# Optimization experiments

Measured on AMD Instinct MI355X. Metric: run time of the kernel, lower is better.

The kernel has to match this reference:

```python
import jax, jax.numpy as jnp
import numpy as np
from jax import lax

B, CIN, COUT, H, W = 4, 256, 256, 64, 64
KH = KW = 3
STRIDE = PAD = DIL = 1
GROUPS = 1
K = KH * KW
HO = (H + 2 * PAD - DIL * (KH - 1) - 1) // STRIDE + 1
WO = (W + 2 * PAD - DIL * (KW - 1) - 1) // STRIDE + 1
DN = ('NCHW', 'OIHW', 'NCHW')


def _sep_conv(x, dw, pw):
    # Separable2d: depthwise kxk conv (stride/pad/dilation) then pointwise 1x1.
    y = lax.conv_general_dilated(x, dw, (STRIDE, STRIDE), [(PAD, PAD), (PAD, PAD)],
                                 rhs_dilation=(DIL, DIL), feature_group_count=x.shape[1],
                                 dimension_numbers=DN)
    return lax.conv_general_dilated(y, pw, (1, 1), 'VALID', dimension_numbers=DN)


def _deform_conv2d(x, offset, mask, weight, bias):
    Bb, Cin, Hh, Ww = x.shape
    O = weight.shape[0]
    G = offset.shape[1] // (2 * K)  # offset groups
    offs = offset.reshape(Bb, G, K, 2, HO, WO)
    dy, dx = offs[:, :, :, 0], offs[:, :, :, 1]  # [B,G,K,Ho,Wo]
    ki, kj = jnp.meshgrid(jnp.arange(KH), jnp.arange(KW), indexing='ij')
    base_y = (-PAD + ki.reshape(K, 1) * DIL + jnp.arange(HO)[None, :] * STRIDE).astype(x.dtype)  # [K,Ho]
    base_x = (-PAD + kj.reshape(K, 1) * DIL + jnp.arange(WO)[None, :] * STRIDE).astype(x.dtype)  # [K,Wo]
    py = base_y[None, None, :, :, None] + dy  # [B,G,K,Ho,Wo]
    px = base_x[None, None, :, None, :] + dx

    xg = x.reshape(Bb, G, Cin // G, Hh, Ww)

    def bilinear(img, py, px):
        # img [C,H,W], py/px [K,Ho,Wo]; zero-padding outside bounds.
        y0 = jnp.floor(py)
        x0 = jnp.floor(px)
        out = jnp.zeros((img.shape[0],) + py.shape, img.dtype)
        for a, (iy, wy) in enumerate((((y0), (y0 + 1 - py)), ((y0 + 1), (py - y0)))):
            for b, (ix, wx) in enumerate((((x0), (x0 + 1 - px)), ((x0 + 1), (px - x0)))):
                valid = (iy >= 0) & (iy < Hh) & (ix >= 0) & (ix < Ww)
                iyc = jnp.clip(iy, 0, Hh - 1).astype(jnp.int32)
                ixc = jnp.clip(ix, 0, Ww - 1).astype(jnp.int32)
                v = img[:, iyc, ixc]  # [C,K,Ho,Wo]
                out = out + v * (wy * wx * valid)[None]
        return out

    sampled = jax.vmap(jax.vmap(bilinear))(xg, py, px)  # [B,G,C/G,K,Ho,Wo]
    m = mask.reshape(Bb, G, K, HO, WO)
    sampled = sampled * m[:, :, None]

    cols = sampled.reshape(Bb, Cin, K, HO, WO).reshape(Bb, GROUPS, Cin // GROUPS, K, HO, WO)
    wr = weight.reshape(GROUPS, O // GROUPS, Cin // GROUPS, K)
    out = jnp.einsum('bgckhw,gock->bgohw', cols, wr).reshape(Bb, O, HO, WO)
    return out + bias[None, :, None, None]


def setup_inputs() -> dict:
    key = jax.random.key(0)
    ks = jax.random.split(key, 7)
    x = jax.random.normal(ks[0], (B, CIN, H, W), jnp.float32)
    weight = jax.random.normal(ks[1], (COUT, CIN // GROUPS, KH, KW), jnp.float32) / np.sqrt(CIN * K)
    bias = jax.random.normal(ks[2], (COUT,), jnp.float32) * 0.01
    off_dw = jax.random.normal(ks[3], (CIN, 1, KH, KW), jnp.float32) * 0.01
    off_pw = jax.random.normal(ks[4], (2 * K * GROUPS, CIN, 1, 1), jnp.float32) * 0.01
    mask_dw = jax.random.normal(ks[5], (CIN, 1, KH, KW), jnp.float32) * 0.01
    mask_pw = jax.random.normal(ks[6], (K * GROUPS, CIN, 1, 1), jnp.float32) * 0.01
    return dict(x=x, weight=weight, bias=bias, off_dw=off_dw, off_pw=off_pw,
                mask_dw=mask_dw, mask_pw=mask_pw)


def reference(x, weight, bias, off_dw, off_pw, mask_dw, mask_pw):
    offset = _sep_conv(x, off_dw, off_pw)                       # [B,2*K,Ho,Wo]
    mask = jax.nn.sigmoid(_sep_conv(x, mask_dw, mask_pw)) * 2.0  # MaskSigmoid(scale=2)
    return _deform_conv2d(x, offset, mask, weight, bias)
```

## Files before the change

kernel.cpp:

```cpp
#include <hip/hip_runtime.h>

#define CIN   256
#define COUT  256
#define HH    64
#define WW    64
#define KD    2304
#define NPIX  16384
#define SPLIT 16
#define CPS   (CIN / SPLIT)
#define NSTEP 36

typedef __attribute__((ext_vector_type(4))) float  float4v;
typedef __attribute__((ext_vector_type(2))) unsigned int uint2v;
typedef _Float16 h2 __attribute__((ext_vector_type(2)));
typedef _Float16 h8 __attribute__((ext_vector_type(8)));
typedef unsigned int u32;
typedef unsigned short u16;

__device__ __forceinline__ h2 as_h2(u32 v) { union { u32 u; h2 h; } x; x.u = v; return x.h; }
__device__ __forceinline__ u32 as_u32(h2 h) { union { u32 u; h2 h; } x; x.h = h; return x.u; }
__device__ __forceinline__ u16 f2h_bits(float f) { _Float16 h = (_Float16)f; return *(u16*)&h; }

__device__ __forceinline__ void gload_lds16(const void* g, void* l) {
  __builtin_amdgcn_global_load_lds((const __attribute__((address_space(1))) u32*)g,
                                   (__attribute__((address_space(3))) u32*)l, 16, 0, 0);
}

__global__ __launch_bounds__(256) void offmask_part_kernel(
    const float* __restrict__ x,
    const float* __restrict__ off_dw, const float* __restrict__ off_pw,
    const float* __restrict__ mask_dw, const float* __restrict__ mask_pw,
    float* __restrict__ part)
{
  int m = blockIdx.x * 256 + threadIdx.x;
  int s = blockIdx.y;
  int b = m >> 12, pix = m & 4095;
  int ho = pix >> 6, wo = pix & 63;
  const float* xb = x + (size_t)b * CIN * 4096;

  float acc[27];
#pragma unroll
  for (int j = 0; j < 27; ++j) acc[j] = 0.f;

  int c0 = s * CPS;
  for (int ci = 0; ci < CPS; ++ci) {
    int c = c0 + ci;
    const float* xc = xb + (size_t)c * 4096;
    float d_off = 0.f, d_msk = 0.f;
#pragma unroll
    for (int t = 0; t < 9; ++t) {
      int gy = ho + t / 3 - 1, gx = wo + t % 3 - 1;
      bool ok = (gy >= 0) & (gy < HH) & (gx >= 0) & (gx < WW);
      float v = ok ? xc[gy * 64 + gx] : 0.f;
      d_off += v * off_dw[c * 9 + t];
      d_msk += v * mask_dw[c * 9 + t];
    }
#pragma unroll
    for (int j = 0; j < 18; ++j) acc[j] += d_off * off_pw[j * 256 + c];
#pragma unroll
    for (int j = 0; j < 9; ++j) acc[18 + j] += d_msk * mask_pw[j * 256 + c];
  }
  float* pp = part + ((size_t)s * NPIX + m) * 32;
#pragma unroll
  for (int j = 0; j < 27; ++j) pp[j] = acc[j];
}

__global__ __launch_bounds__(256) void offmask_reduce_kernel(
    const float* __restrict__ part, float* __restrict__ rec)
{
  int i = blockIdx.x * 256 + threadIdx.x;
  int m = i >> 5, j = i & 31;
  if (j >= 27) { rec[i] = 0.f; return; }
  float sum = 0.f;
#pragma unroll
  for (int s = 0; s < SPLIT; ++s) sum += part[((size_t)s * NPIX + m) * 32 + j];
  rec[i] = (j < 18) ? sum : 2.f / (1.f + __expf(-sum));
}

__global__ __launch_bounds__(256) void wconv_kernel(const float* __restrict__ w,
                                                    u16* __restrict__ wb)
{
  int i = blockIdx.x * 256 + threadIdx.x;
  int co = i / KD, rem = i - co * KD;
  int c = rem / 9, kk = rem - c * 9;
  wb[co * KD + kk * 256 + c] = f2h_bits(w[i]);
}

__global__ __launch_bounds__(256) void xpose_kernel(const float* __restrict__ x,
                                                    u16* __restrict__ xt)
{
  __shared__ float t[64][65];
  int ptile = blockIdx.x;
  int ctile = blockIdx.y;
  int b     = blockIdx.z;
  int tid = threadIdx.x;
  const float* xb = x + (size_t)b * CIN * 4096 + (size_t)ctile * 64 * 4096 + ptile * 64;
#pragma unroll
  for (int i = 0; i < 16; ++i) {
    int c = i * 4 + (tid >> 6), p = tid & 63;
    t[c][p] = xb[(size_t)c * 4096 + p];
  }
  __syncthreads();
  u16* xo = xt + ((size_t)b * 4096 + ptile * 64) * 256 + ctile * 64;
#pragma unroll
  for (int i = 0; i < 16; ++i) {
    int p = i * 4 + (tid >> 6), c = tid & 63;
    xo[(size_t)p * 256 + c] = f2h_bits(t[c][p]);
  }
}

__global__ __launch_bounds__(512, 4) void gemm_fused_kernel(
    const u16* __restrict__ A,
    const u16* __restrict__ xt,
    const float* __restrict__ rec,
    const float* __restrict__ bias,
    float* __restrict__ out,
    float* __restrict__ tmp)
{
  __shared__ __align__(16) u16 lA[3][256 * 32];
  __shared__ __align__(16) u16 lB[2][64 * 32];
  const int tid = threadIdx.x;
  const int bid = blockIdx.x;
  const int h   = bid & 1;
  const int ptile = bid >> 1;
  const int m0  = ptile * 64;
  const int b_img = ptile >> 6;
  const int cbase = h * 128;
  const int wave = tid >> 6, lane = tid & 63;
  const int wm = wave >> 1, wn = wave & 1;
  const int rl = lane & 15, kq = lane >> 4;
  const int sA = (kq ^ (rl & 3) ^ ((rl >> 2) & 3)) * 8;

  const int rA  = tid >> 2;
  const int koA = ((tid & 3) ^ (rA & 3) ^ ((rA >> 2) & 3)) * 8;
  const u16* aRow0 = A + (size_t)rA * KD + koA;
  const u16* aRow1 = A + (size_t)(rA + 128) * KD + koA;

  const int spx = tid >> 3;
  const int sc4 = (tid & 7) * 4;
  const int m_px = m0 + spx;
  const int ho = (m_px & 4095) >> 6, wo = m_px & 63;
  const float* rp = rec + (size_t)m_px * 32;
  const u16* xb = xt + (size_t)b_img * 4096 * 256;
  const int wAddr = spx * 32 +
                    ((((tid >> 1) & 3) ^ ((spx & 3) ^ ((spx >> 2) & 3))) * 8) +
                    (tid & 1) * 4;

  u32 cOff[4];
  h2  wh[4];

#define KCOL(t_) (((t_) >> 2) * 256 + cbase + ((t_) & 3) * 32)

#define CALC_CORNERS(kk_) do {                                             \
    float dy = rp[(kk_) * 2], dx = rp[(kk_) * 2 + 1], msk = rp[18 + (kk_)];\
    float py  = (float)(ho - 1 + ((kk_) / 3)) + dy;                        \
    float pxf = (float)(wo - 1 + ((kk_) % 3)) + dx;                        \
    float fy = floorf(py), fx = floorf(pxf);                               \
    int y0 = (int)fy, x0 = (int)fx;                                        \
    float wy1 = py - fy, wy0 = 1.f - wy1;                                  \
    float wx1 = pxf - fx, wx0 = 1.f - wx1;                                 \
    _Pragma("unroll")                                                      \
    for (int cr = 0; cr < 4; ++cr) {                                       \
      int iy = y0 + (cr >> 1), ix = x0 + (cr & 1);                         \
      bool valid = (iy >= 0) & (iy < HH) & (ix >= 0) & (ix < WW);          \
      int iyc = min(max(iy, 0), HH - 1), ixc = min(max(ix, 0), WW - 1);    \
      cOff[cr] = (u32)(iyc * 64 + ixc) * 256;                              \
      float wy = (cr >> 1) ? wy1 : wy0;                                    \
      float wx = (cr & 1) ? wx1 : wx0;                                     \
      float wf = valid ? (wy * wx * msk) : 0.f;                            \
      _Float16 hw = (_Float16)wf;                                          \
      wh[cr] = (h2){hw, hw};                                               \
    }                                                                      \
  } while (0)

#define STAGE_A(k_, slot_) do {                                            \
    int k0_ = KCOL(k_);                                                    \
    gload_lds16(aRow0 + k0_, lA[slot_] + tid * 8);                         \
    gload_lds16(aRow1 + k0_, lA[slot_] + (tid + 512) * 8);                 \
  } while (0)

#define BLEND_WRITE(bufi_, v0_, v1_, v2_, v3_) do {                        \
    h2 a01 = wh[0] * as_h2((v0_)[0]) + wh[1] * as_h2((v1_)[0]);            \
    a01   += wh[2] * as_h2((v2_)[0]) + wh[3] * as_h2((v3_)[0]);            \
    h2 a23 = wh[0] * as_h2((v0_)[1]) + wh[1] * as_h2((v1_)[1]);            \
    a23   += wh[2] * as_h2((v2_)[1]) + wh[3] * as_h2((v3_)[1]);            \
    uint2v wv; wv[0] = as_u32(a01); wv[1] = as_u32(a23);                   \
    *(uint2v*)&lB[bufi_][wAddr] = wv;                                      \
  } while (0)

  float4v acc[4][2];
#pragma unroll
  for (int m = 0; m < 4; ++m)
#pragma unroll
    for (int n = 0; n < 2; ++n) acc[m][n] = float4v{0.f, 0.f, 0.f, 0.f};

  {
    CALC_CORNERS(0);
    int c0n = cbase + sc4;
    uint2v v0 = *(const uint2v*)(xb + cOff[0] + c0n);
    uint2v v1 = *(const uint2v*)(xb + cOff[1] + c0n);
    uint2v v2 = *(const uint2v*)(xb + cOff[2] + c0n);
    uint2v v3 = *(const uint2v*)(xb + cOff[3] + c0n);
    STAGE_A(0, 0);
    STAGE_A(1, 1);
    asm volatile("s_waitcnt vmcnt(2)" ::: "memory");
    BLEND_WRITE(0, v0, v1, v2, v3);
    asm volatile("s_waitcnt lgkmcnt(0)" ::: "memory");
    __builtin_amdgcn_s_barrier();
  }

  for (int it = 0; it < 6; ++it) {
#pragma unroll
    for (int u = 0; u < 6; ++u) {
      const int t = it * 6 + u;
      const int tn  = (t + 1 == NSTEP) ? 0 : t + 1;
      const int tn2 = (t + 2 >= NSTEP) ? (t + 2 - NSTEP) : t + 2;
      if ((tn & 3) == 0) CALC_CORNERS(tn >> 2);
      int c0n = cbase + (tn & 3) * 32 + sc4;
      uint2v v0 = *(const uint2v*)(xb + cOff[0] + c0n);
      uint2v v1 = *(const uint2v*)(xb + cOff[1] + c0n);
      uint2v v2 = *(const uint2v*)(xb + cOff[2] + c0n);
      uint2v v3 = *(const uint2v*)(xb + cOff[3] + c0n);
      STAGE_A(tn2, (u + 2) % 3);
      h8 af[4], bf[2];
#pragma unroll
      for (int m = 0; m < 4; ++m)
        af[m] = *(const h8*)&lA[u % 3][(wm * 64 + m * 16 + rl) * 32 + sA];
#pragma unroll
      for (int n = 0; n < 2; ++n)
        bf[n] = *(const h8*)&lB[u & 1][(wn * 32 + n * 16 + rl) * 32 + sA];
#pragma unroll
      for (int m = 0; m < 4; ++m)
#pragma unroll
        for (int n = 0; n < 2; ++n)
          acc[m][n] = __builtin_amdgcn_mfma_f32_16x16x32_f16(af[m], bf[n], acc[m][n], 0, 0, 0);
      asm volatile("s_waitcnt vmcnt(2)" ::: "memory");
      BLEND_WRITE((u + 1) & 1, v0, v1, v2, v3);
      asm volatile("s_waitcnt lgkmcnt(0)" ::: "memory");
      __builtin_amdgcn_s_barrier();
    }
  }
#undef STAGE_A
#undef CALC_CORNERS
#undef BLEND_WRITE
#undef KCOL

  const int p_base = (m0 & 4095) + wn * 32;
  float* db = (h ? tmp : out) + (size_t)b_img * COUT * 4096;
#pragma unroll
  for (int m = 0; m < 4; ++m) {
#pragma unroll
    for (int j = 0; j < 4; ++j) {
      int co = wm * 64 + m * 16 + kq * 4 + j;
      float bv = h ? 0.f : bias[co];
#pragma unroll
      for (int n = 0; n < 2; ++n) {
        int pp = p_base + n * 16 + rl;
        db[(size_t)co * 4096 + pp] = acc[m][n][j] + bv;
      }
    }
  }
}

__global__ __launch_bounds__(256) void add_kernel(float* __restrict__ out,
                                                  const float* __restrict__ tmp)
{
  size_t i = ((size_t)blockIdx.x * 256 + threadIdx.x) * 4;
  float4v a = *(const float4v*)(out + i);
  float4v b = *(const float4v*)(tmp + i);
  a += b;
  *(float4v*)(out + i) = a;
}

extern "C" void kernel_launch(void* const* d_in, const int* in_sizes, int n_in,
                              void* d_out, int out_size, void* d_ws, size_t ws_size,
                              hipStream_t stream) {
  const float* x       = (const float*)d_in[0];
  const float* weight  = (const float*)d_in[1];
  const float* bias    = (const float*)d_in[2];
  const float* off_dw  = (const float*)d_in[3];
  const float* off_pw  = (const float*)d_in[4];
  const float* mask_dw = (const float*)d_in[5];
  const float* mask_pw = (const float*)d_in[6];

  if (ws_size < 45219840ull) return;
  float* rec  = (float*)d_ws;
  u16*   wb   = (u16*)((char*)d_ws + 2097152);
  u16*   xt   = (u16*)((char*)d_ws + 3276800);
  float* part = (float*)((char*)d_ws + 11665408);
  float* tmp  = part;
  float* out  = (float*)d_out;

  wconv_kernel<<<dim3(2304), dim3(256), 0, stream>>>(weight, wb);
  offmask_part_kernel<<<dim3(NPIX / 256, SPLIT), dim3(256), 0, stream>>>(
      x, off_dw, off_pw, mask_dw, mask_pw, part);
  offmask_reduce_kernel<<<dim3(NPIX * 32 / 256), dim3(256), 0, stream>>>(part, rec);
  xpose_kernel<<<dim3(64, 4, 4), dim3(256), 0, stream>>>(x, xt);
  gemm_fused_kernel<<<dim3(512), dim3(512), 0, stream>>>(wb, xt, rec, bias, out, tmp);
  add_kernel<<<dim3(COUT * NPIX / 4 / 256), dim3(256), 0, stream>>>(out, tmp);
}
```

Baseline: 107.1 us.

## Enlarge GEMM pixel tile to 256 and split K four ways

Each GEMM block now covers 256 pixels instead of 64, with the channel range split four ways (64 channels per block) rather than two. Each A-tile load from LDS is reused across 8 MFMA column tiles instead of 2, and the bilinear sampling loads use 16-byte vectors. This raises arithmetic intensity per staged weight tile and halves the grid to 256 blocks. In exchange it uses more accumulator registers (occupancy hint dropped to 2), more LDS, and three partial-sum buffers that add_kernel must read and reduce, which adds global traffic.

```diff
diff --git a/kernel.cpp b/kernel.cpp
--- a/kernel.cpp
+++ b/kernel.cpp
@@ -8,10 +8,10 @@
 #define NPIX  16384
 #define SPLIT 16
 #define CPS   (CIN / SPLIT)
-#define NSTEP 36
+#define NSTEP 18
 
 typedef __attribute__((ext_vector_type(4))) float  float4v;
-typedef __attribute__((ext_vector_type(2))) unsigned int uint2v;
+typedef __attribute__((ext_vector_type(4))) unsigned int uint4v;
 typedef _Float16 h2 __attribute__((ext_vector_type(2)));
 typedef _Float16 h8 __attribute__((ext_vector_type(8)));
 typedef unsigned int u32;
@@ -109,7 +109,7 @@
   }
 }
 
-__global__ __launch_bounds__(512, 4) void gemm_fused_kernel(
+__global__ __launch_bounds__(512, 2) void gemm_fused_kernel(
     const u16* __restrict__ A,
     const u16* __restrict__ xt,
     const float* __restrict__ rec,
@@ -118,14 +118,14 @@
     float* __restrict__ tmp)
 {
   __shared__ __align__(16) u16 lA[3][256 * 32];
-  __shared__ __align__(16) u16 lB[2][64 * 32];
+  __shared__ __align__(16) u16 lB[2][256 * 32];
   const int tid = threadIdx.x;
   const int bid = blockIdx.x;
-  const int h   = bid & 1;
-  const int ptile = bid >> 1;
-  const int m0  = ptile * 64;
-  const int b_img = ptile >> 6;
-  const int cbase = h * 128;
+  const int h   = bid & 3;
+  const int ptile = bid >> 2;
+  const int m0  = ptile * 256;
+  const int b_img = ptile >> 4;
+  const int cbase = h * 64;
   const int wave = tid >> 6, lane = tid & 63;
   const int wm = wave >> 1, wn = wave & 1;
   const int rl = lane & 15, kq = lane >> 4;
@@ -136,20 +136,20 @@
   const u16* aRow0 = A + (size_t)rA * KD + koA;
   const u16* aRow1 = A + (size_t)(rA + 128) * KD + koA;
 
-  const int spx = tid >> 3;
-  const int sc4 = (tid & 7) * 4;
-  const int m_px = m0 + spx;
+  const int px_t = tid >> 1;
+  const int chh  = (tid & 1) * 16;
+  const int m_px = m0 + px_t;
   const int ho = (m_px & 4095) >> 6, wo = m_px & 63;
   const float* rp = rec + (size_t)m_px * 32;
   const u16* xb = xt + (size_t)b_img * 4096 * 256;
-  const int wAddr = spx * 32 +
-                    ((((tid >> 1) & 3) ^ ((spx & 3) ^ ((spx >> 2) & 3))) * 8) +
-                    (tid & 1) * 4;
+  const int swzp = (px_t & 3) ^ ((px_t >> 2) & 3);
+  const int wAddr0 = px_t * 32 + ((((tid & 1) * 2)     ^ swzp) * 8);
+  const int wAddr1 = px_t * 32 + ((((tid & 1) * 2 + 1) ^ swzp) * 8);
 
   u32 cOff[4];
   h2  wh[4];
 
-#define KCOL(t_) (((t_) >> 2) * 256 + cbase + ((t_) & 3) * 32)
+#define KCOL(t_) (((t_) >> 1) * 256 + cbase + ((t_) & 1) * 32)
 
 #define CALC_CORNERS(kk_) do {                                             \
     float dy = rp[(kk_) * 2], dx = rp[(kk_) * 2 + 1], msk = rp[18 + (kk_)];\
@@ -179,74 +179,84 @@
     gload_lds16(aRow1 + k0_, lA[slot_] + (tid + 512) * 8);                 \
   } while (0)
 
-#define BLEND_WRITE(bufi_, v0_, v1_, v2_, v3_) do {                        \
-    h2 a01 = wh[0] * as_h2((v0_)[0]) + wh[1] * as_h2((v1_)[0]);            \
-    a01   += wh[2] * as_h2((v2_)[0]) + wh[3] * as_h2((v3_)[0]);            \
-    h2 a23 = wh[0] * as_h2((v0_)[1]) + wh[1] * as_h2((v1_)[1]);            \
-    a23   += wh[2] * as_h2((v2_)[1]) + wh[3] * as_h2((v3_)[1]);            \
-    uint2v wv; wv[0] = as_u32(a01); wv[1] = as_u32(a23);                   \
-    *(uint2v*)&lB[bufi_][wAddr] = wv;                                      \
+#define SAMP_LOAD(t_, va, vb) do {                                         \
+    int c0n_ = cbase + ((t_) & 1) * 32 + chh;                              \
+    _Pragma("unroll")                                                      \
+    for (int cr = 0; cr < 4; ++cr) {                                       \
+      va[cr] = *(const uint4v*)(xb + cOff[cr] + c0n_);                     \
+      vb[cr] = *(const uint4v*)(xb + cOff[cr] + c0n_ + 8);                 \
+    }                                                                      \
   } while (0)
 
-  float4v acc[4][2];
+#define BLEND_WRITE(bufi_, va, vb) do {                                    \
+    uint4v o0, o1;                                                         \
+    _Pragma("unroll")                                                      \
+    for (int w_ = 0; w_ < 4; ++w_) {                                       \
+      h2 s0_ = wh[0] * as_h2(va[0][w_]) + wh[1] * as_h2(va[1][w_]);        \
+      s0_   += wh[2] * as_h2(va[2][w_]) + wh[3] * as_h2(va[3][w_]);        \
+      h2 s1_ = wh[0] * as_h2(vb[0][w_]) + wh[1] * as_h2(vb[1][w_]);        \
+      s1_   += wh[2] * as_h2(vb[2][w_]) + wh[3] * as_h2(vb[3][w_]);        \
+      o0[w_] = as_u32(s0_); o1[w_] = as_u32(s1_);                          \
+    }                                                                      \
+    *(uint4v*)&lB[bufi_][wAddr0] = o0;                                     \
+    *(uint4v*)&lB[bufi_][wAddr1] = o1;                                     \
+  } while (0)
+
+  float4v acc[4][8];
 #pragma unroll
   for (int m = 0; m < 4; ++m)
 #pragma unroll
-    for (int n = 0; n < 2; ++n) acc[m][n] = float4v{0.f, 0.f, 0.f, 0.f};
+    for (int n = 0; n < 8; ++n) acc[m][n] = float4v{0.f, 0.f, 0.f, 0.f};
 
   {
     CALC_CORNERS(0);
-    int c0n = cbase + sc4;
-    uint2v v0 = *(const uint2v*)(xb + cOff[0] + c0n);
-    uint2v v1 = *(const uint2v*)(xb + cOff[1] + c0n);
-    uint2v v2 = *(const uint2v*)(xb + cOff[2] + c0n);
-    uint2v v3 = *(const uint2v*)(xb + cOff[3] + c0n);
+    uint4v va[4], vb[4];
+    SAMP_LOAD(0, va, vb);
     STAGE_A(0, 0);
     STAGE_A(1, 1);
     asm volatile("s_waitcnt vmcnt(2)" ::: "memory");
-    BLEND_WRITE(0, v0, v1, v2, v3);
+    BLEND_WRITE(0, va, vb);
     asm volatile("s_waitcnt lgkmcnt(0)" ::: "memory");
     __builtin_amdgcn_s_barrier();
   }
 
-  for (int it = 0; it < 6; ++it) {
+  for (int it = 0; it < 3; ++it) {
 #pragma unroll
     for (int u = 0; u < 6; ++u) {
       const int t = it * 6 + u;
       const int tn  = (t + 1 == NSTEP) ? 0 : t + 1;
       const int tn2 = (t + 2 >= NSTEP) ? (t + 2 - NSTEP) : t + 2;
-      if ((tn & 3) == 0) CALC_CORNERS(tn >> 2);
-      int c0n = cbase + (tn & 3) * 32 + sc4;
-      uint2v v0 = *(const uint2v*)(xb + cOff[0] + c0n);
-      uint2v v1 = *(const uint2v*)(xb + cOff[1] + c0n);
-      uint2v v2 = *(const uint2v*)(xb + cOff[2] + c0n);
-      uint2v v3 = *(const uint2v*)(xb + cOff[3] + c0n);
+      if ((tn & 1) == 0) CALC_CORNERS(tn >> 1);
+      uint4v va[4], vb[4];
+      SAMP_LOAD(tn, va, vb);
       STAGE_A(tn2, (u + 2) % 3);
-      h8 af[4], bf[2];
+      h8 af[4], bf[8];
 #pragma unroll
       for (int m = 0; m < 4; ++m)
         af[m] = *(const h8*)&lA[u % 3][(wm * 64 + m * 16 + rl) * 32 + sA];
 #pragma unroll
-      for (int n = 0; n < 2; ++n)
-        bf[n] = *(const h8*)&lB[u & 1][(wn * 32 + n * 16 + rl) * 32 + sA];
+      for (int n = 0; n < 8; ++n)
+        bf[n] = *(const h8*)&lB[u & 1][(wn * 128 + n * 16 + rl) * 32 + sA];
 #pragma unroll
       for (int m = 0; m < 4; ++m)
 #pragma unroll
-        for (int n = 0; n < 2; ++n)
+        for (int n = 0; n < 8; ++n)
           acc[m][n] = __builtin_amdgcn_mfma_f32_16x16x32_f16(af[m], bf[n], acc[m][n], 0, 0, 0);
       asm volatile("s_waitcnt vmcnt(2)" ::: "memory");
-      BLEND_WRITE((u + 1) & 1, v0, v1, v2, v3);
+      BLEND_WRITE((u + 1) & 1, va, vb);
       asm volatile("s_waitcnt lgkmcnt(0)" ::: "memory");
       __builtin_amdgcn_s_barrier();
     }
   }
 #undef STAGE_A
 #undef CALC_CORNERS
+#undef SAMP_LOAD
 #undef BLEND_WRITE
 #undef KCOL
 
-  const int p_base = (m0 & 4095) + wn * 32;
-  float* db = (h ? tmp : out) + (size_t)b_img * COUT * 4096;
+  const int p_base = (m0 & 4095) + wn * 128;
+  float* db = (h ? (tmp + (size_t)(h - 1) * COUT * NPIX) : out) +
+              (size_t)b_img * COUT * 4096;
 #pragma unroll
   for (int m = 0; m < 4; ++m) {
 #pragma unroll
@@ -254,7 +264,7 @@
       int co = wm * 64 + m * 16 + kq * 4 + j;
       float bv = h ? 0.f : bias[co];
 #pragma unroll
-      for (int n = 0; n < 2; ++n) {
+      for (int n = 0; n < 8; ++n) {
         int pp = p_base + n * 16 + rl;
         db[(size_t)co * 4096 + pp] = acc[m][n][j] + bv;
       }
@@ -266,9 +276,11 @@
                                                   const float* __restrict__ tmp)
 {
   size_t i = ((size_t)blockIdx.x * 256 + threadIdx.x) * 4;
-  float4v a = *(const float4v*)(out + i);
-  float4v b = *(const float4v*)(tmp + i);
-  a += b;
+  float4v a  = *(const float4v*)(out + i);
+  float4v b0 = *(const float4v*)(tmp + i);
+  float4v b1 = *(const float4v*)(tmp + (size_t)COUT * NPIX + i);
+  float4v b2 = *(const float4v*)(tmp + (size_t)2 * COUT * NPIX + i);
+  a += b0 + b1 + b2;
   *(float4v*)(out + i) = a;
 }
 
@@ -283,7 +295,7 @@
   const float* mask_dw = (const float*)d_in[5];
   const float* mask_pw = (const float*)d_in[6];
 
-  if (ws_size < 45219840ull) return;
+  if (ws_size < 61997056ull) return;
   float* rec  = (float*)d_ws;
   u16*   wb   = (u16*)((char*)d_ws + 2097152);
   u16*   xt   = (u16*)((char*)d_ws + 3276800);
@@ -296,6 +308,6 @@
       x, off_dw, off_pw, mask_dw, mask_pw, part);
   offmask_reduce_kernel<<<dim3(NPIX * 32 / 256), dim3(256), 0, stream>>>(part, rec);
   xpose_kernel<<<dim3(64, 4, 4), dim3(256), 0, stream>>>(x, xt);
-  gemm_fused_kernel<<<dim3(512), dim3(512), 0, stream>>>(wb, xt, rec, bias, out, tmp);
+  gemm_fused_kernel<<<dim3(256), dim3(512), 0, stream>>>(wb, xt, rec, bias, out, tmp);
   add_kernel<<<dim3(COUT * NPIX / 4 / 256), dim3(256), 0, stream>>>(out, tmp);
 }
```

New measurement: 107.1 us. No clear change (+0.0%).

## Double GEMM pixel tile to 128 and remap blocks across XCDs

Applied to the files above, without the earlier changes.

The fused deformable-sampling GEMM now covers 128 pixels per block instead of 64. Each thread gathers 8 channels per corner with 16-byte loads, and each wave computes a 4x4 grid of MFMA tiles. Block IDs are remapped so that the two channel halves of a pixel tile land on the same XCD. The goal is to reuse each staged weight tile across twice as many pixels and cut A-matrix traffic. The cost is more accumulator registers and only 256 blocks, which lowers occupancy and the number of CUs kept busy.

```diff
diff --git a/kernel.cpp b/kernel.cpp
--- a/kernel.cpp
+++ b/kernel.cpp
@@ -11,7 +11,7 @@
 #define NSTEP 36
 
 typedef __attribute__((ext_vector_type(4))) float  float4v;
-typedef __attribute__((ext_vector_type(2))) unsigned int uint2v;
+typedef __attribute__((ext_vector_type(4))) unsigned int uint4v;
 typedef _Float16 h2 __attribute__((ext_vector_type(2)));
 typedef _Float16 h8 __attribute__((ext_vector_type(8)));
 typedef unsigned int u32;
@@ -118,13 +118,14 @@
     float* __restrict__ tmp)
 {
   __shared__ __align__(16) u16 lA[3][256 * 32];
-  __shared__ __align__(16) u16 lB[2][64 * 32];
+  __shared__ __align__(16) u16 lB[2][128 * 32];
   const int tid = threadIdx.x;
-  const int bid = blockIdx.x;
-  const int h   = bid & 1;
-  const int ptile = bid >> 1;
-  const int m0  = ptile * 64;
-  const int b_img = ptile >> 6;
+  const int ord = blockIdx.x;
+  const int xcd = ord & 7, slot = ord >> 3;
+  const int ptile = (slot >> 1) * 8 + xcd;
+  const int h     = slot & 1;
+  const int m0  = ptile * 128;
+  const int b_img = ptile >> 5;
   const int cbase = h * 128;
   const int wave = tid >> 6, lane = tid & 63;
   const int wm = wave >> 1, wn = wave & 1;
@@ -136,15 +137,14 @@
   const u16* aRow0 = A + (size_t)rA * KD + koA;
   const u16* aRow1 = A + (size_t)(rA + 128) * KD + koA;
 
-  const int spx = tid >> 3;
-  const int sc4 = (tid & 7) * 4;
-  const int m_px = m0 + spx;
+  const int px_t = tid >> 2;
+  const int ch8  = (tid & 3) * 8;
+  const int m_px = m0 + px_t;
   const int ho = (m_px & 4095) >> 6, wo = m_px & 63;
   const float* rp = rec + (size_t)m_px * 32;
   const u16* xb = xt + (size_t)b_img * 4096 * 256;
-  const int wAddr = spx * 32 +
-                    ((((tid >> 1) & 3) ^ ((spx & 3) ^ ((spx >> 2) & 3))) * 8) +
-                    (tid & 1) * 4;
+  const int swzp = (px_t & 3) ^ ((px_t >> 2) & 3);
+  const int wAddr = px_t * 32 + (((tid & 3) ^ swzp) * 8);
 
   u32 cOff[4];
   h2  wh[4];
@@ -179,73 +179,77 @@
     gload_lds16(aRow1 + k0_, lA[slot_] + (tid + 512) * 8);                 \
   } while (0)
 
-#define BLEND_WRITE(bufi_, v0_, v1_, v2_, v3_) do {                        \
-    h2 a01 = wh[0] * as_h2((v0_)[0]) + wh[1] * as_h2((v1_)[0]);            \
-    a01   += wh[2] * as_h2((v2_)[0]) + wh[3] * as_h2((v3_)[0]);            \
-    h2 a23 = wh[0] * as_h2((v0_)[1]) + wh[1] * as_h2((v1_)[1]);            \
-    a23   += wh[2] * as_h2((v2_)[1]) + wh[3] * as_h2((v3_)[1]);            \
-    uint2v wv; wv[0] = as_u32(a01); wv[1] = as_u32(a23);                   \
-    *(uint2v*)&lB[bufi_][wAddr] = wv;                                      \
+#define SAMP_LOAD(t_, va) do {                                             \
+    int c0n_ = cbase + ((t_) & 3) * 32 + ch8;                              \
+    _Pragma("unroll")                                                      \
+    for (int cr = 0; cr < 4; ++cr)                                         \
+      va[cr] = *(const uint4v*)(xb + cOff[cr] + c0n_);                     \
   } while (0)
 
-  float4v acc[4][2];
+#define BLEND_WRITE(bufi_, va) do {                                        \
+    uint4v o0;                                                             \
+    _Pragma("unroll")                                                      \
+    for (int w_ = 0; w_ < 4; ++w_) {                                       \
+      h2 s0_ = wh[0] * as_h2(va[0][w_]) + wh[1] * as_h2(va[1][w_]);        \
+      s0_   += wh[2] * as_h2(va[2][w_]) + wh[3] * as_h2(va[3][w_]);        \
+      o0[w_] = as_u32(s0_);                                                \
+    }                                                                      \
+    *(uint4v*)&lB[bufi_][wAddr] = o0;                                      \
+  } while (0)
+
+  float4v acc[4][4];
 #pragma unroll
   for (int m = 0; m < 4; ++m)
 #pragma unroll
-    for (int n = 0; n < 2; ++n) acc[m][n] = float4v{0.f, 0.f, 0.f, 0.f};
+    for (int n = 0; n < 4; ++n) acc[m][n] = float4v{0.f, 0.f, 0.f, 0.f};
 
   {
     CALC_CORNERS(0);
-    int c0n = cbase + sc4;
-    uint2v v0 = *(const uint2v*)(xb + cOff[0] + c0n);
-    uint2v v1 = *(const uint2v*)(xb + cOff[1] + c0n);
-    uint2v v2 = *(const uint2v*)(xb + cOff[2] + c0n);
-    uint2v v3 = *(const uint2v*)(xb + cOff[3] + c0n);
+    uint4v va[4];
+    SAMP_LOAD(0, va);
     STAGE_A(0, 0);
     STAGE_A(1, 1);
     asm volatile("s_waitcnt vmcnt(2)" ::: "memory");
-    BLEND_WRITE(0, v0, v1, v2, v3);
+    BLEND_WRITE(0, va);
     asm volatile("s_waitcnt lgkmcnt(0)" ::: "memory");
     __builtin_amdgcn_s_barrier();
   }
 
-  for (int it = 0; it < 6; ++it) {
-#pragma unroll
-    for (int u = 0; u < 6; ++u) {
-      const int t = it * 6 + u;
+  for (int it = 0; it < 3; ++it) {
+#pragma unroll
+    for (int u = 0; u < 12; ++u) {
+      const int t = it * 12 + u;
       const int tn  = (t + 1 == NSTEP) ? 0 : t + 1;
       const int tn2 = (t + 2 >= NSTEP) ? (t + 2 - NSTEP) : t + 2;
       if ((tn & 3) == 0) CALC_CORNERS(tn >> 2);
-      int c0n = cbase + (tn & 3) * 32 + sc4;
-      uint2v v0 = *(const uint2v*)(xb + cOff[0] + c0n);
-      uint2v v1 = *(const uint2v*)(xb + cOff[1] + c0n);
-      uint2v v2 = *(const uint2v*)(xb + cOff[2] + c0n);
-      uint2v v3 = *(const uint2v*)(xb + cOff[3] + c0n);
+      uint4v va[4];
+      SAMP_LOAD(tn, va);
       STAGE_A(tn2, (u + 2) % 3);
-      h8 af[4], bf[2];
+      h8 af[4], bf[4];
 #pragma unroll
       for (int m = 0; m < 4; ++m)
         af[m] = *(const h8*)&lA[u % 3][(wm * 64 + m * 16 + rl) * 32 + sA];
 #pragma unroll
-      for (int n = 0; n < 2; ++n)
-        bf[n] = *(const h8*)&lB[u & 1][(wn * 32 + n * 16 + rl) * 32 + sA];
+      for (int n = 0; n < 4; ++n)
+        bf[n] = *(const h8*)&lB[u & 1][(wn * 64 + n * 16 + rl) * 32 + sA];
 #pragma unroll
       for (int m = 0; m < 4; ++m)
 #pragma unroll
-        for (int n = 0; n < 2; ++n)
+        for (int n = 0; n < 4; ++n)
           acc[m][n] = __builtin_amdgcn_mfma_f32_16x16x32_f16(af[m], bf[n], acc[m][n], 0, 0, 0);
       asm volatile("s_waitcnt vmcnt(2)" ::: "memory");
-      BLEND_WRITE((u + 1) & 1, v0, v1, v2, v3);
+      BLEND_WRITE((u + 1) & 1, va);
       asm volatile("s_waitcnt lgkmcnt(0)" ::: "memory");
       __builtin_amdgcn_s_barrier();
     }
   }
 #undef STAGE_A
 #undef CALC_CORNERS
+#undef SAMP_LOAD
 #undef BLEND_WRITE
 #undef KCOL
 
-  const int p_base = (m0 & 4095) + wn * 32;
+  const int p_base = (m0 & 4095) + wn * 64;
   float* db = (h ? tmp : out) + (size_t)b_img * COUT * 4096;
 #pragma unroll
   for (int m = 0; m < 4; ++m) {
@@ -254,7 +258,7 @@
       int co = wm * 64 + m * 16 + kq * 4 + j;
       float bv = h ? 0.f : bias[co];
 #pragma unroll
-      for (int n = 0; n < 2; ++n) {
+      for (int n = 0; n < 4; ++n) {
         int pp = p_base + n * 16 + rl;
         db[(size_t)co * 4096 + pp] = acc[m][n][j] + bv;
       }
@@ -296,6 +300,6 @@
       x, off_dw, off_pw, mask_dw, mask_pw, part);
   offmask_reduce_kernel<<<dim3(NPIX * 32 / 256), dim3(256), 0, stream>>>(part, rec);
   xpose_kernel<<<dim3(64, 4, 4), dim3(256), 0, stream>>>(x, xt);
-  gemm_fused_kernel<<<dim3(512), dim3(512), 0, stream>>>(wb, xt, rec, bias, out, tmp);
+  gemm_fused_kernel<<<dim3(256), dim3(512), 0, stream>>>(wb, xt, rec, bias, out, tmp);
   add_kernel<<<dim3(COUT * NPIX / 4 / 256), dim3(256), 0, stream>>>(out, tmp);
 }
```

New measurement: 125.8 us. 17.5% more time.
